# Optimization experiments

Measured on AMD Instinct MI355X. Metric: run time of the kernel, lower is better.

Reference implementation:

```python
import jax, jax.numpy as jnp
import numpy as np

B, T, K = 256, 1024, 128  # batch, seq_len, num_tags (= config.vocab_size)


def setup_inputs() -> dict:
    key = jax.random.key(0)
    k1, k2, k3, k4 = jax.random.split(key, 4)
    return {
        "hidden_states": jax.random.normal(k1, (B, T, K), dtype=jnp.float32),
        "transitions": jax.random.normal(k2, (K, K), dtype=jnp.float32) * 0.1,
        "start_transitions": jax.random.normal(k3, (K,), dtype=jnp.float32) * 0.1,
        "end_transitions": jax.random.normal(k4, (K,), dtype=jnp.float32) * 0.1,
    }


def reference(hidden_states, transitions, start_transitions, end_transitions):
    """CRF forward algorithm: log-partition over all tag sequences.

    hidden_states: [B, T, K] emission scores
    transitions:   [K, K]  transitions[i, j] = score of tag i -> tag j
    Returns logZ per sequence: [B]
    """
    emis = hidden_states
    # alpha_0: [B, K]
    alpha0 = start_transitions[None, :] + emis[:, 0]

    def step(alpha, e_t):
        # alpha: [B, K] log-scores ending at previous tag
        # scores[b, i, j] = alpha[b, i] + transitions[i, j]
        scores = alpha[:, :, None] + transitions[None, :, :]  # [B, K, K]
        new_alpha = jax.nn.logsumexp(scores, axis=1) + e_t    # [B, K]
        return new_alpha, None

    emis_rest = jnp.swapaxes(emis[:, 1:], 0, 1)  # [T-1, B, K]
    alphaT, _ = jax.lax.scan(step, alpha0, emis_rest)
    return jax.nn.logsumexp(alphaT + end_transitions[None, :], axis=1)  # [B]
```

## Files before the change

kernel.cpp:

```cpp
#include <hip/hip_runtime.h>
#include <cstddef>
#include <cstdint>

typedef float f32x4 __attribute__((ext_vector_type(4)));
typedef short bf16x8 __attribute__((ext_vector_type(8)));

__device__ __forceinline__ float fast_exp2(float x) { return __builtin_amdgcn_exp2f(x); }
__device__ __forceinline__ float fast_log2(float x) { return __builtin_amdgcn_logf(x); }

__device__ __forceinline__ short bf16rne(float x) {
  uint32_t u = __float_as_uint(x);
  u += 0x7fffu + ((u >> 16) & 1u);
  return (short)(u >> 16);
}

namespace {
constexpr int Bc = 256, Tc = 1024, Kc = 128;
constexpr int NC = 96;
constexpr int WARM = 12;
constexpr int MEAS = 1023 - WARM;
constexpr float L2E = 1.4426950408889634f;
constexpr float LN2 = 0.6931471805599453f;
constexpr int WS_ET2 = NC * Bc;
}

__global__ __launch_bounds__(128, 1) void crf_prep(
    const float* __restrict__ trans, float* __restrict__ ws)
{
  unsigned short* et = reinterpret_cast<unsigned short*>(ws + WS_ET2);
  const int m = (int)blockIdx.x;
  const int c = (int)threadIdx.x;
  const int tau = (c & 0x63) | ((c & 4) << 2) | ((c & 0x18) >> 1);
  et[(size_t)m * Kc + c] =
      (unsigned short)bf16rne(fast_exp2(trans[(size_t)tau * Kc + m] * L2E));
}

__global__ __launch_bounds__(64) void crf_chunk_kernel(
    const float* __restrict__ hs,
    const float* __restrict__ start_t,
    const float* __restrict__ end_t,
    float* __restrict__ ws)
{
  const int lane = (int)threadIdx.x;
  const int b = lane & 15;
  const int q = lane >> 4;
  const int rb = (int)blockIdx.x & 15;
  const int ck = (int)blockIdx.x >> 4;
  const int brow = rb * 16 + b;
  const int s0 = (MEAS * ck) / NC;
  const int L  = (MEAS * (ck + 1)) / NC - s0;
  const int NSTEPS = WARM + L;
  const float* __restrict__ eb = hs + (size_t)brow * Tc * Kc + (size_t)s0 * Kc;
  const unsigned short* __restrict__ et =
      reinterpret_cast<const unsigned short*>(ws + WS_ET2);

  bf16x8 Ap[8][4];
#pragma unroll
  for (int nt = 0; nt < 8; ++nt)
#pragma unroll
    for (int tt = 0; tt < 4; ++tt)
      Ap[nt][tt] = *(const bf16x8*)&et[(size_t)(16 * nt + b) * Kc + 32 * tt + 8 * q];

  f32x4 er[8];
#pragma unroll
  for (int nt = 0; nt < 8; ++nt)
    er[nt] = *(const f32x4*)&eb[(size_t)Kc + 16 * nt + 4 * q];

  bf16x8 Bf[4];
  if (ck == 0) {
#pragma unroll
    for (int tt = 0; tt < 4; ++tt) {
      f32x4 sv0 = *(const f32x4*)&start_t[32 * tt + 4 * q];
      f32x4 sv1 = *(const f32x4*)&start_t[32 * tt + 4 * q + 16];
      f32x4 e0v = *(const f32x4*)&eb[32 * tt + 4 * q];
      f32x4 e1v = *(const f32x4*)&eb[32 * tt + 4 * q + 16];
      bf16x8 v;
      v[0] = bf16rne(fast_exp2((sv0.x + e0v.x) * L2E));
      v[1] = bf16rne(fast_exp2((sv0.y + e0v.y) * L2E));
      v[2] = bf16rne(fast_exp2((sv0.z + e0v.z) * L2E));
      v[3] = bf16rne(fast_exp2((sv0.w + e0v.w) * L2E));
      v[4] = bf16rne(fast_exp2((sv1.x + e1v.x) * L2E));
      v[5] = bf16rne(fast_exp2((sv1.y + e1v.y) * L2E));
      v[6] = bf16rne(fast_exp2((sv1.z + e1v.z) * L2E));
      v[7] = bf16rne(fast_exp2((sv1.w + e1v.w) * L2E));
      Bf[tt] = v;
    }
  } else {
    const short one = (short)0x3F80;
#pragma unroll
    for (int tt = 0; tt < 4; ++tt) {
      bf16x8 v;
#pragma unroll
      for (int j = 0; j < 8; ++j) v[j] = one;
      Bf[tt] = v;
    }
  }

  float sf = 0.f;
  int curE0 = 0;
  int Mi = 0;
  f32x4 P[8];

#define STEP(T) do {                                                            \
    const f32x4 z4 = {0.f, 0.f, 0.f, 0.f};                                      \
    Mi += curE0;                                                                \
    float c00src = 0.f;                                                         \
    _Pragma("unroll")                                                           \
    for (int nt = 0; nt < 8; ++nt) {                                            \
      f32x4 c01 = __builtin_amdgcn_mfma_f32_16x16x32_bf16(Ap[nt][1], Bf[1],     \
          __builtin_amdgcn_mfma_f32_16x16x32_bf16(Ap[nt][0], Bf[0], z4, 0, 0, 0), \
          0, 0, 0);                                                             \
      f32x4 c23 = __builtin_amdgcn_mfma_f32_16x16x32_bf16(Ap[nt][3], Bf[3],     \
          __builtin_amdgcn_mfma_f32_16x16x32_bf16(Ap[nt][2], Bf[2], z4, 0, 0, 0), \
          0, 0, 0);                                                             \
      f32x4 cv = c01 + c23;                                                     \
      if (nt == 0) c00src = cv.x;                                               \
      f32x4 e = er[nt];                                                         \
      f32x4 p;                                                                  \
      p.x = cv.x * fast_exp2(__builtin_fmaf(e.x, L2E, sf));                     \
      p.y = cv.y * fast_exp2(__builtin_fmaf(e.y, L2E, sf));                     \
      p.z = cv.z * fast_exp2(__builtin_fmaf(e.z, L2E, sf));                     \
      p.w = cv.w * fast_exp2(__builtin_fmaf(e.w, L2E, sf));                     \
      P[nt] = p;                                                                \
    }                                                                           \
    {                                                                           \
      int rn = (T) + 1; if (rn > NSTEPS) rn = NSTEPS;                           \
      _Pragma("unroll")                                                         \
      for (int nt = 0; nt < 8; ++nt)                                            \
        er[nt] = *(const f32x4*)&eb[(size_t)rn * Kc + 16 * nt + 4 * q];         \
    }                                                                           \
    float c00 = __shfl(c00src, b, 64);   \
    _Pragma("unroll")                                                           \
    for (int tt = 0; tt < 4; ++tt) {                                            \
      bf16x8 v;                                                                 \
      v[0] = bf16rne(P[2 * tt].x);     v[1] = bf16rne(P[2 * tt].y);             \
      v[2] = bf16rne(P[2 * tt].z);     v[3] = bf16rne(P[2 * tt].w);             \
      v[4] = bf16rne(P[2 * tt + 1].x); v[5] = bf16rne(P[2 * tt + 1].y);         \
      v[6] = bf16rne(P[2 * tt + 1].z); v[7] = bf16rne(P[2 * tt + 1].w);         \
      Bf[tt] = v;                                                               \
    }                                                                           \
    {                                                                           \
      uint32_t ex = (__float_as_uint(c00) >> 23) & 0xffu;                       \
      curE0 = (int)ex - 127;                                                    \
      sf = (float)(127 - (int)ex);                                              \
    }                                                                           \
  } while (0)

#define MEASURE(DST, WEIGHTED) do {                                             \
    float part = 0.f;                                                           \
    if (WEIGHTED) {                                                             \
      _Pragma("unroll")                                                         \
      for (int nt = 0; nt < 8; ++nt) {                                          \
        f32x4 ev = *(const f32x4*)&end_t[16 * nt + 4 * q];                      \
        part += P[nt].x * fast_exp2(ev.x * L2E) + P[nt].y * fast_exp2(ev.y * L2E) \
              + P[nt].z * fast_exp2(ev.z * L2E) + P[nt].w * fast_exp2(ev.w * L2E); \
      }                                                                         \
    } else {                                                                    \
      _Pragma("unroll")                                                         \
      for (int nt = 0; nt < 8; ++nt)                                            \
        part += P[nt].x + P[nt].y + P[nt].z + P[nt].w;                          \
    }                                                                           \
    part += __shfl_xor(part, 16);                                               \
    part += __shfl_xor(part, 32);                                               \
    DST = (float)Mi + fast_log2(part);                                          \
  } while (0)

  STEP(1);  STEP(2);  STEP(3);  STEP(4);
  STEP(5);  STEP(6);  STEP(7);  STEP(8);
  STEP(9);  STEP(10); STEP(11); STEP(12);
  float Amid; MEASURE(Amid, false);

  STEP(13); STEP(14); STEP(15); STEP(16);
  STEP(17); STEP(18); STEP(19); STEP(20);
  STEP(21); STEP(22);
  if (L == 11) { STEP(23); }
  float Aend; MEASURE(Aend, (ck == NC - 1));

#undef STEP
#undef MEASURE

  if (lane < 16)
    ws[(size_t)ck * Bc + brow] = Aend - (ck ? Amid : 0.f);
}

__global__ __launch_bounds__(256, 1) void crf_combine(
    const float* __restrict__ ws, float* __restrict__ out)
{
  const int b = (int)threadIdx.x;
  float s = 0.f;
#pragma unroll
  for (int cc = 0; cc < NC; ++cc) s += ws[(size_t)cc * Bc + b];
  out[b] = s * LN2;
}

extern "C" void kernel_launch(void* const* d_in, const int* in_sizes, int n_in,
                              void* d_out, int out_size, void* d_ws, size_t ws_size,
                              hipStream_t stream) {
  const float* hs    = (const float*)d_in[0];
  const float* trans = (const float*)d_in[1];
  const float* st    = (const float*)d_in[2];
  const float* en    = (const float*)d_in[3];
  float* ws = (float*)d_ws;
  crf_prep<<<dim3(Kc), dim3(Kc), 0, stream>>>(trans, ws);
  crf_chunk_kernel<<<dim3(NC * 16), dim3(64), 0, stream>>>(hs, st, en, ws);
  crf_combine<<<dim3(1), dim3(Bc), 0, stream>>>(ws, (float*)d_out);
}
```

Before: 224.0 us.

## Prefetch emissions via async global-to-LDS ring buffer three steps ahead

Replaces the per-step direct global loads of emission rows into registers with a three-slot LDS ring buffer filled by global_load_lds, issued three steps ahead. Loads are coalesced per row and stored with an XOR swizzle to avoid bank conflicts, and explicit vmcnt/lgkmcnt waits gate the reads. The aim is to hide global memory latency on the serial recurrence chain. In exchange it adds LDS traffic, manual waitcnt management and fragile ordering assumptions.

```diff
diff --git a/kernel.cpp b/kernel.cpp
--- a/kernel.cpp
+++ b/kernel.cpp
@@ -41,9 +41,15 @@
     const float* __restrict__ end_t,
     float* __restrict__ ws)
 {
+  __shared__ __align__(16) float ering[3][2048];
+
   const int lane = (int)threadIdx.x;
   const int b = lane & 15;
   const int q = lane >> 4;
+  const int b7 = b & 7;
+  const int h = lane >> 5;
+  const int w31 = lane & 31;
+  const int wh = w31 ^ h;
   const int rb = (int)blockIdx.x & 15;
   const int ck = (int)blockIdx.x >> 4;
   const int brow = rb * 16 + b;
@@ -51,6 +57,8 @@
   const int L  = (MEAS * (ck + 1)) / NC - s0;
   const int NSTEPS = WARM + L;
   const float* __restrict__ eb = hs + (size_t)brow * Tc * Kc + (size_t)s0 * Kc;
+  const float* __restrict__ pbase =
+      hs + (size_t)(rb * 16 + h) * (Tc * Kc) + (size_t)s0 * Kc;
   const unsigned short* __restrict__ et =
       reinterpret_cast<const unsigned short*>(ws + WS_ET2);
 
@@ -60,11 +68,6 @@
 #pragma unroll
     for (int tt = 0; tt < 4; ++tt)
       Ap[nt][tt] = *(const bf16x8*)&et[(size_t)(16 * nt + b) * Kc + 32 * tt + 8 * q];
-
-  f32x4 er[8];
-#pragma unroll
-  for (int nt = 0; nt < 8; ++nt)
-    er[nt] = *(const f32x4*)&eb[(size_t)Kc + 16 * nt + 4 * q];
 
   bf16x8 Bf[4];
   if (ck == 0) {
@@ -99,9 +102,33 @@
   float sf = 0.f;
   int curE0 = 0;
   int Mi = 0;
+  f32x4 er[8];
   f32x4 P[8];
 
+#define RING_ISSUE(RN_, SL_) do {                                               \
+    int rn_ = (RN_); if (rn_ > NSTEPS) rn_ = NSTEPS;                            \
+    _Pragma("unroll")                                                           \
+    for (int nt = 0; nt < 8; ++nt) {                                            \
+      const float* src_ = pbase + (size_t)(2 * nt) * (Tc * Kc)                  \
+                        + (size_t)rn_ * Kc + (size_t)((wh ^ ((2 * nt) & 7)) * 4); \
+      __builtin_amdgcn_global_load_lds(                                         \
+          (const __attribute__((address_space(1))) uint32_t*)(const void*)src_, \
+          (__attribute__((address_space(3))) uint32_t*)(void*)&ering[SL_][nt * 256], \
+          16, 0, 0);                                                            \
+    }                                                                           \
+  } while (0)
+
+#define RING_READ(T1_) do {                                                     \
+    asm volatile("s_waitcnt vmcnt(16)" ::: "memory");                           \
+    const float* rp_ = &ering[(T1_) % 3][0];                                    \
+    _Pragma("unroll")                                                           \
+    for (int nt = 0; nt < 8; ++nt)                                              \
+      er[nt] = *(const f32x4*)&rp_[b * 128 + (((4 * nt + q) ^ b7) * 4)];        \
+  } while (0)
+
 #define STEP(T) do {                                                            \
+    asm volatile("s_waitcnt lgkmcnt(0)" ::: "memory");                          \
+    RING_ISSUE((T) + 3, (T) % 3);                                               \
     const f32x4 z4 = {0.f, 0.f, 0.f, 0.f};                                      \
     Mi += curE0;                                                                \
     float c00src = 0.f;                                                         \
@@ -123,13 +150,7 @@
       p.w = cv.w * fast_exp2(__builtin_fmaf(e.w, L2E, sf));                     \
       P[nt] = p;                                                                \
     }                                                                           \
-    {                                                                           \
-      int rn = (T) + 1; if (rn > NSTEPS) rn = NSTEPS;                           \
-      _Pragma("unroll")                                                         \
-      for (int nt = 0; nt < 8; ++nt)                                            \
-        er[nt] = *(const f32x4*)&eb[(size_t)rn * Kc + 16 * nt + 4 * q];         \
-    }                                                                           \
-    float c00 = __shfl(c00src, b, 64);   \
+    float c00 = __shfl(c00src, b, 64);              \
     _Pragma("unroll")                                                           \
     for (int tt = 0; tt < 4; ++tt) {                                            \
       bf16x8 v;                                                                 \
@@ -144,6 +165,7 @@
       curE0 = (int)ex - 127;                                                    \
       sf = (float)(127 - (int)ex);                                              \
     }                                                                           \
+    RING_READ((T) + 1);                                                         \
   } while (0)
 
 #define MEASURE(DST, WEIGHTED) do {                                             \
@@ -165,6 +187,11 @@
     DST = (float)Mi + fast_log2(part);                                          \
   } while (0)
 
+  RING_ISSUE(1, 1);
+  RING_ISSUE(2, 2);
+  RING_ISSUE(3, 0);
+  RING_READ(1);
+
   STEP(1);  STEP(2);  STEP(3);  STEP(4);
   STEP(5);  STEP(6);  STEP(7);  STEP(8);
   STEP(9);  STEP(10); STEP(11); STEP(12);
@@ -178,6 +205,8 @@
 
 #undef STEP
 #undef MEASURE
+#undef RING_ISSUE
+#undef RING_READ
 
   if (lane < 16)
     ws[(size_t)ck * Bc + brow] = Aend - (ck ? Amid : 0.f);
```

Result: slower. 229.7 us (+2.6%).

## Cut chunk count and prefetch emissions through an LDS ring via global_load_lds

Applied to the files above, without the earlier changes.

Splits the sequence into 32 chunks instead of 96, so each block runs about 43 steps and repeats the 12-step warm-up less often. Emission rows are no longer loaded straight into registers one step ahead. They are now fetched asynchronously into a 4-slot shared-memory ring several steps ahead, using direct global-to-LDS loads and explicit vmcnt waits. The goal is to hide global load latency behind the serial MFMA recurrence and cut redundant warm-up work. The cost is fewer blocks (512 instead of 1536), which lowers parallelism on the GPU, plus hand-tuned waitcnt bookkeeping that is fragile.

```diff
diff --git a/kernel.cpp b/kernel.cpp
--- a/kernel.cpp
+++ b/kernel.cpp
@@ -16,7 +16,7 @@
 
 namespace {
 constexpr int Bc = 256, Tc = 1024, Kc = 128;
-constexpr int NC = 96;
+constexpr int NC = 32;
 constexpr int WARM = 12;
 constexpr int MEAS = 1023 - WARM;
 constexpr float L2E = 1.4426950408889634f;
@@ -41,16 +41,21 @@
     const float* __restrict__ end_t,
     float* __restrict__ ws)
 {
+  __shared__ __align__(16) float ering[4][16][256];
+
   const int lane = (int)threadIdx.x;
   const int b = lane & 15;
   const int q = lane >> 4;
+  const int b7 = b & 7;
+  const int h2v = (lane >> 5) * 128;
+  const int s31 = lane & 31;
   const int rb = (int)blockIdx.x & 15;
   const int ck = (int)blockIdx.x >> 4;
   const int brow = rb * 16 + b;
   const int s0 = (MEAS * ck) / NC;
   const int L  = (MEAS * (ck + 1)) / NC - s0;
-  const int NSTEPS = WARM + L;
   const float* __restrict__ eb = hs + (size_t)brow * Tc * Kc + (size_t)s0 * Kc;
+  const float* __restrict__ hb = hs + (size_t)(rb * 16) * (Tc * Kc) + (size_t)s0 * Kc;
   const unsigned short* __restrict__ et =
       reinterpret_cast<const unsigned short*>(ws + WS_ET2);
 
@@ -60,11 +65,6 @@
 #pragma unroll
     for (int tt = 0; tt < 4; ++tt)
       Ap[nt][tt] = *(const bf16x8*)&et[(size_t)(16 * nt + b) * Kc + 32 * tt + 8 * q];
-
-  f32x4 er[8];
-#pragma unroll
-  for (int nt = 0; nt < 8; ++nt)
-    er[nt] = *(const f32x4*)&eb[(size_t)Kc + 16 * nt + 4 * q];
 
   bf16x8 Bf[4];
   if (ck == 0) {
@@ -99,9 +99,38 @@
   float sf = 0.f;
   int curE0 = 0;
   int Mi = 0;
+  f32x4 er[8];
   f32x4 P[8];
 
+#define RING_ISSUE(RR) do {                                                     \
+    constexpr int Rp_ = ((RR) > 43) ? 43 : (RR);                                \
+    constexpr int pr_ = (((RR) + 1) >> 1) & 3;                                  \
+    _Pragma("unroll")                                                           \
+    for (int i = 0; i < 16; ++i) {                                              \
+      const float* src_ = hb + (size_t)i * (Tc * Kc) + (size_t)Rp_ * Kc         \
+                        + (size_t)(h2v + ((s31 ^ (i & 7)) << 2));               \
+      __builtin_amdgcn_global_load_lds(                                         \
+          (const __attribute__((address_space(1))) uint32_t*)(const void*)src_, \
+          (__attribute__((address_space(3))) uint32_t*)(void*)&ering[pr_][i][0],\
+          16, 0, 0);                                                            \
+    }                                                                           \
+  } while (0)
+
+#define RING_READ(R1, VC) do {                                                  \
+    asm volatile("s_waitcnt vmcnt(" #VC ")" ::: "memory");                      \
+    constexpr int prr_ = (((R1) + 1) >> 1) & 3;                                 \
+    constexpr int hf_ = ((R1) + 1) & 1;                                         \
+    const float* rp_ = &ering[prr_][0][0];                                      \
+    _Pragma("unroll")                                                           \
+    for (int nt = 0; nt < 8; ++nt)                                              \
+      er[nt] = *(const f32x4*)&rp_[b * 256 + hf_ * 128 + (((4 * nt + q) ^ b7) << 2)]; \
+  } while (0)
+
 #define STEP(T) do {                                                            \
+    if ((T) & 1) {                                                              \
+      asm volatile("s_waitcnt lgkmcnt(0)" ::: "memory");                        \
+      RING_ISSUE((T) + 6);                                                      \
+    }                                                                           \
     const f32x4 z4 = {0.f, 0.f, 0.f, 0.f};                                      \
     Mi += curE0;                                                                \
     float c00src = 0.f;                                                         \
@@ -123,13 +152,7 @@
       p.w = cv.w * fast_exp2(__builtin_fmaf(e.w, L2E, sf));                     \
       P[nt] = p;                                                                \
     }                                                                           \
-    {                                                                           \
-      int rn = (T) + 1; if (rn > NSTEPS) rn = NSTEPS;                           \
-      _Pragma("unroll")                                                         \
-      for (int nt = 0; nt < 8; ++nt)                                            \
-        er[nt] = *(const f32x4*)&eb[(size_t)rn * Kc + 16 * nt + 4 * q];         \
-    }                                                                           \
-    float c00 = __shfl(c00src, b, 64);   \
+    float c00 = __shfl(c00src, b, 64);              \
     _Pragma("unroll")                                                           \
     for (int tt = 0; tt < 4; ++tt) {                                            \
       bf16x8 v;                                                                 \
@@ -144,6 +167,7 @@
       curE0 = (int)ex - 127;                                                    \
       sf = (float)(127 - (int)ex);                                              \
     }                                                                           \
+    if ((T) & 1) { RING_READ((T) + 1, 48); } else { RING_READ((T) + 1, 32); }   \
   } while (0)
 
 #define MEASURE(DST, WEIGHTED) do {                                             \
@@ -165,6 +189,11 @@
     DST = (float)Mi + fast_log2(part);                                          \
   } while (0)
 
+  RING_ISSUE(1);
+  RING_ISSUE(3);
+  RING_ISSUE(5);
+  RING_READ(1, 32);
+
   STEP(1);  STEP(2);  STEP(3);  STEP(4);
   STEP(5);  STEP(6);  STEP(7);  STEP(8);
   STEP(9);  STEP(10); STEP(11); STEP(12);
@@ -172,12 +201,19 @@
 
   STEP(13); STEP(14); STEP(15); STEP(16);
   STEP(17); STEP(18); STEP(19); STEP(20);
-  STEP(21); STEP(22);
-  if (L == 11) { STEP(23); }
+  STEP(21); STEP(22); STEP(23); STEP(24);
+  STEP(25); STEP(26); STEP(27); STEP(28);
+  STEP(29); STEP(30); STEP(31); STEP(32);
+  STEP(33); STEP(34); STEP(35); STEP(36);
+  STEP(37); STEP(38); STEP(39); STEP(40);
+  STEP(41); STEP(42); STEP(43);
+  if (L == 32) { STEP(44); }
   float Aend; MEASURE(Aend, (ck == NC - 1));
 
 #undef STEP
 #undef MEASURE
+#undef RING_ISSUE
+#undef RING_READ
 
   if (lane < 16)
     ws[(size_t)ck * Bc + brow] = Aend - (ck ? Amid : 0.f);
```

After: 234.5 us. +4.7%, slower.
